# Optimization experiments

Hardware: AMD Instinct MI355X
Metric: run time of the kernel (lower is better)

## Reference

```python
import jax, jax.numpy as jnp
import numpy as np

EMBED_DIM = 512
NUM_HEADS = 8
HEAD_DIM = EMBED_DIM // NUM_HEADS


def setup_inputs() -> dict:
    key = jax.random.key(0)
    ks = jax.random.split(key, 6)
    B, S, D = 2, 4096, EMBED_DIM
    scale = 1.0 / np.sqrt(D)
    inputs = jax.random.normal(ks[0], (B, S, D), dtype=jnp.float32)
    Wq = jax.random.normal(ks[1], (D, D), dtype=jnp.float32) * scale
    Wk = jax.random.normal(ks[2], (D, D), dtype=jnp.float32) * scale
    Wv = jax.random.normal(ks[3], (D, D), dtype=jnp.float32) * scale
    Wo = jax.random.normal(ks[4], (D, D), dtype=jnp.float32) * scale
    zeros = jnp.zeros((D,), dtype=jnp.float32)
    return {"inputs": inputs, "Wq": Wq, "bq": zeros, "Wk": Wk, "bk": zeros,
            "Wv": Wv, "bv": zeros, "Wo": Wo, "bo": zeros}


def _split_heads(x, B, S):
    # [B,S,D] -> [B,H,S,hd]
    return x.reshape(B, S, NUM_HEADS, HEAD_DIM).transpose(0, 2, 1, 3)


def reference(inputs, Wq, bq, Wk, bk, Wv, bv, Wo, bo):
    B, S, D = inputs.shape
    q = _split_heads(inputs @ Wq + bq, B, S)
    k = _split_heads(inputs @ Wk + bk, B, S)
    v = _split_heads(inputs @ Wv + bv, B, S)
    scale = 1.0 / jnp.sqrt(jnp.asarray(HEAD_DIM, dtype=inputs.dtype))
    # full [B,H,S,S] score matrix, as in the original naive SDPA
    scores = jnp.einsum('bhqd,bhkd->bhqk', q, k) * scale
    weights = jax.nn.softmax(scores, axis=-1)
    attn = jnp.einsum('bhqk,bhkd->bhqd', weights, v)
    attn = attn.transpose(0, 2, 1, 3).reshape(B, S, D)
    return attn @ Wo + bo
```

## Files before the change

### kernel.cpp

```cpp
#include <hip/hip_runtime.h>
#include <hip/hip_bf16.h>
#include <stdint.h>


typedef __bf16 bf16x8 __attribute__((ext_vector_type(8)));
typedef float f32x4 __attribute__((ext_vector_type(4)));

using as1_void = __attribute__((address_space(1))) void;
using as3_void = __attribute__((address_space(3))) void;

__device__ __forceinline__ void gload16(const void* g, void* l) {
    __builtin_amdgcn_global_load_lds((const as1_void*)g, (as3_void*)l, 16, 0, 0);
}

__device__ __forceinline__ f32x4 mfma16(bf16x8 a, bf16x8 b, f32x4 c) {
    return __builtin_amdgcn_mfma_f32_16x16x32_bf16(a, b, c, 0, 0, 0);
}

__device__ __forceinline__ uint32_t pkbf(float a, float b) {
    union { __hip_bfloat16 h[2]; uint32_t u; } r;
    r.h[0] = __float2bfloat16(a);
    r.h[1] = __float2bfloat16(b);
    return r.u;
}

__global__ void cvt_x(const float* __restrict__ in, __hip_bfloat16* __restrict__ out, int n) {
    int i = (blockIdx.x * 256 + threadIdx.x) * 4;
    if (i >= n) return;
    float4 v = *reinterpret_cast<const float4*>(in + i);
    union { __hip_bfloat16 h[4]; uint2 u; } r;
    r.h[0] = __float2bfloat16(v.x);
    r.h[1] = __float2bfloat16(v.y);
    r.h[2] = __float2bfloat16(v.z);
    r.h[3] = __float2bfloat16(v.w);
    *reinterpret_cast<uint2*>(out + i) = r.u;
}

__global__ void cvt_wt(const float* __restrict__ w0, const float* __restrict__ w1,
                       const float* __restrict__ w2, const float* __restrict__ w3,
                       __hip_bfloat16* __restrict__ o0, __hip_bfloat16* __restrict__ o1,
                       __hip_bfloat16* __restrict__ o2, __hip_bfloat16* __restrict__ o3) {
    const float* W; __hip_bfloat16* O;
    switch (blockIdx.z) {
        case 0: W = w0; O = o0; break;
        case 1: W = w1; O = o1; break;
        case 2: W = w2; O = o2; break;
        default: W = w3; O = o3; break;
    }
    __shared__ float t[32][33];
    int n0 = blockIdx.x * 32, k0 = blockIdx.y * 32;
    int tx = threadIdx.x, ty = threadIdx.y;
    for (int j = 0; j < 4; ++j)
        t[ty + 8 * j][tx] = W[(size_t)(k0 + ty + 8 * j) * 512 + n0 + tx];
    __syncthreads();
    for (int j = 0; j < 4; ++j)
        O[(size_t)(n0 + ty + 8 * j) * 512 + k0 + tx] = __float2bfloat16(t[tx][ty + 8 * j]);
}

__global__ __launch_bounds__(256, 2) void gemm_qkv(
    const __hip_bfloat16* __restrict__ A, const __hip_bfloat16* __restrict__ Bt,
    const float* __restrict__ bq, const float* __restrict__ bk, const float* __restrict__ bv,
    __hip_bfloat16* __restrict__ Qb, __hip_bfloat16* __restrict__ Kb,
    __hip_bfloat16* __restrict__ Vtb, float qs)
{
    const int K = 512;
    __shared__ __hip_bfloat16 Abuf[128 * 32];
    __shared__ __hip_bfloat16 Bbuf[128 * 32];
    const int tid = threadIdx.x, w = tid >> 6, lane = tid & 63;
    const int col = lane & 15, quad = lane >> 4;
    const int wr = w >> 1, wc = w & 1;
    const int tileN = blockIdx.x * 128, tileM = blockIdx.y * 128;

    f32x4 acc[4][4] = {};

    for (int k0 = 0; k0 < K; k0 += 32) {
        for (int i = 0; i < 2; ++i) {
            int g = w * 2 + i;
            int chunk = g * 64 + lane;
            int row = chunk >> 2, c8 = chunk & 3;
            gload16(A + (size_t)(tileM + row) * K + k0 + c8 * 8, Abuf + g * 512);
            gload16(Bt + (size_t)(tileN + row) * K + k0 + c8 * 8, Bbuf + g * 512);
        }
        __syncthreads();
        bf16x8 af[4], bfr[4];
        for (int mt = 0; mt < 4; ++mt)
            af[mt] = *reinterpret_cast<const bf16x8*>(Abuf + (wr * 64 + mt * 16 + col) * 32 + quad * 8);
        for (int nt = 0; nt < 4; ++nt)
            bfr[nt] = *reinterpret_cast<const bf16x8*>(Bbuf + (wc * 64 + nt * 16 + col) * 32 + quad * 8);
        for (int mt = 0; mt < 4; ++mt)
            for (int nt = 0; nt < 4; ++nt)
                acc[mt][nt] = mfma16(af[mt], bfr[nt], acc[mt][nt]);
        __syncthreads();
    }

    const int seg = (tileN + wc * 64) >> 9;
    const float* bias = (seg == 0) ? bq : (seg == 1) ? bk : bv;
    const float scale = (seg == 0) ? qs : 1.0f;
    __hip_bfloat16* outp = (seg == 0) ? Qb : (seg == 1) ? Kb : Vtb;

    for (int mt = 0; mt < 4; ++mt) {
        for (int nt = 0; nt < 4; ++nt) {
            int n = tileN + wc * 64 + nt * 16 + col;
            int nn = n & 511, h = nn >> 6, d = nn & 63;
            float bn = bias[nn];
            for (int r = 0; r < 4; ++r) {
                int m = tileM + wr * 64 + mt * 16 + quad * 4 + r;
                int b = m >> 12, s = m & 4095;
                float v = (acc[mt][nt][r] + bn) * scale;
                size_t off;
                if (seg < 2) off = (((size_t)(b * 8 + h) * 4096 + s) << 6) + d;
                else         off = (((size_t)(b * 8 + h) * 64 + d) << 12) + s;
                outp[off] = __float2bfloat16(v);
            }
        }
    }
}

__global__ __launch_bounds__(256, 2) void gemm_out(
    const __hip_bfloat16* __restrict__ A, const __hip_bfloat16* __restrict__ Bt,
    const float* __restrict__ bias, float* __restrict__ out)
{
    const int N = 512, K = 512;
    __shared__ __hip_bfloat16 Abuf[128 * 32];
    __shared__ __hip_bfloat16 Bbuf[128 * 32];
    const int tid = threadIdx.x, w = tid >> 6, lane = tid & 63;
    const int col = lane & 15, quad = lane >> 4;
    const int wr = w >> 1, wc = w & 1;
    const int tileN = blockIdx.x * 128, tileM = blockIdx.y * 128;

    f32x4 acc[4][4] = {};

    for (int k0 = 0; k0 < K; k0 += 32) {
        for (int i = 0; i < 2; ++i) {
            int g = w * 2 + i;
            int chunk = g * 64 + lane;
            int row = chunk >> 2, c8 = chunk & 3;
            gload16(A + (size_t)(tileM + row) * K + k0 + c8 * 8, Abuf + g * 512);
            gload16(Bt + (size_t)(tileN + row) * K + k0 + c8 * 8, Bbuf + g * 512);
        }
        __syncthreads();
        bf16x8 af[4], bfr[4];
        for (int mt = 0; mt < 4; ++mt)
            af[mt] = *reinterpret_cast<const bf16x8*>(Abuf + (wr * 64 + mt * 16 + col) * 32 + quad * 8);
        for (int nt = 0; nt < 4; ++nt)
            bfr[nt] = *reinterpret_cast<const bf16x8*>(Bbuf + (wc * 64 + nt * 16 + col) * 32 + quad * 8);
        for (int mt = 0; mt < 4; ++mt)
            for (int nt = 0; nt < 4; ++nt)
                acc[mt][nt] = mfma16(af[mt], bfr[nt], acc[mt][nt]);
        __syncthreads();
    }

    for (int mt = 0; mt < 4; ++mt) {
        for (int nt = 0; nt < 4; ++nt) {
            int n = tileN + wc * 64 + nt * 16 + col;
            float bn = bias[n];
            for (int r = 0; r < 4; ++r) {
                int m = tileM + wr * 64 + mt * 16 + quad * 4 + r;
                out[(size_t)m * N + n] = acc[mt][nt][r] + bn;
            }
        }
    }
}

__global__ __launch_bounds__(256) void flash(
    const __hip_bfloat16* __restrict__ Q,
    const __hip_bfloat16* __restrict__ Kq,
    const __hip_bfloat16* __restrict__ Vt,
    __hip_bfloat16* __restrict__ attnb)
{
    __shared__ __hip_bfloat16 KT[2][4096];
    __shared__ __hip_bfloat16 VB[2][4096];
    __shared__ uint32_t TB[4][1024];

    const int bh = blockIdx.y, b = bh >> 3, h = bh & 7;
    const int tid = threadIdx.x, w = tid >> 6, lane = tid & 63;
    const int col = lane & 15, quad = lane >> 4;
    const int q0 = blockIdx.x * 128 + w * 32;
    const int c7 = col & 7;

    const __hip_bfloat16* Qh = Q + (size_t)bh * 4096 * 64;
    const __hip_bfloat16* Kh = Kq + (size_t)bh * 4096 * 64;
    const __hip_bfloat16* Vh = Vt + (size_t)bh * 64 * 4096;

    bf16x8 aq[2][2];
    for (int qh = 0; qh < 2; ++qh)
        for (int ks = 0; ks < 2; ++ks)
            aq[qh][ks] = *reinterpret_cast<const bf16x8*>(
                Qh + (size_t)(q0 + qh * 16 + col) * 64 + ks * 32 + quad * 8);

    const __hip_bfloat16* ksrc[2];
    const __hip_bfloat16* vsrc[2];
    int ldsoff[2];
    for (int i = 0; i < 2; ++i) {
        int c = i * 256 + tid;
        int row = c >> 3, s8 = (c & 7) ^ (row & 7);
        ksrc[i] = Kh + row * 64 + s8 * 8;
        vsrc[i] = Vh + (size_t)row * 4096 + s8 * 8;
        ldsoff[i] = (i * 256 + w * 64) * 8;
    }

    bf16x8 ones;
    for (int j = 0; j < 8; ++j) ones[j] = (__bf16)1.0f;

    f32x4 o[4][2] = {};
    f32x4 accl[2] = {};

    uint32_t* TBw = &TB[w][0];

    for (int i = 0; i < 2; ++i) {
        gload16(ksrc[i], &KT[0][ldsoff[i]]);
        gload16(vsrc[i], &VB[0][ldsoff[i]]);
    }
    __syncthreads();

    for (int kt = 0; kt < 64; ++kt) {
        const int p = kt & 1;
        if (kt < 63) {
            for (int i = 0; i < 2; ++i) {
                gload16(ksrc[i] + (size_t)(kt + 1) * 4096, &KT[1 - p][ldsoff[i]]);
                gload16(vsrc[i] + (size_t)(kt + 1) * 64,   &VB[1 - p][ldsoff[i]]);
            }
        }

        f32x4 sc[4][2] = {};
        for (int ks = 0; ks < 2; ++ks)
            for (int kg = 0; kg < 4; ++kg) {
                bf16x8 ak = *reinterpret_cast<const bf16x8*>(
                    &KT[p][(kg * 16 + col) * 64 + (((ks * 4 + quad) ^ c7) << 3)]);
                for (int qh = 0; qh < 2; ++qh)
                    sc[kg][qh] = mfma16(ak, aq[qh][ks], sc[kg][qh]);
            }

        for (int kg = 0; kg < 4; ++kg)
            for (int qh = 0; qh < 2; ++qh) {
                f32x4 v = sc[kg][qh];
                uint32_t u0 = pkbf(__builtin_amdgcn_exp2f(v[0]), __builtin_amdgcn_exp2f(v[1]));
                uint32_t u1 = pkbf(__builtin_amdgcn_exp2f(v[2]), __builtin_amdgcn_exp2f(v[3]));
                int q = qh * 16 + col;
                int base = q * 32 + (((kg * 2 + (quad >> 1)) ^ c7) << 2) + ((quad & 1) * 2);
                TBw[base]     = u0;
                TBw[base + 1] = u1;
            }

        bf16x8 bp[2][2];
        for (int qh = 0; qh < 2; ++qh)
            for (int ks = 0; ks < 2; ++ks) {
                int q = qh * 16 + col;
                bp[qh][ks] = *reinterpret_cast<const bf16x8*>(
                    &TBw[q * 32 + (((ks * 4 + quad) ^ c7) << 2)]);
            }

        for (int ks = 0; ks < 2; ++ks) {
            for (int dt = 0; dt < 4; ++dt) {
                bf16x8 av = *reinterpret_cast<const bf16x8*>(
                    &VB[p][(dt * 16 + col) * 64 + (((ks * 4 + quad) ^ c7) << 3)]);
                for (int qh = 0; qh < 2; ++qh)
                    o[dt][qh] = mfma16(av, bp[qh][ks], o[dt][qh]);
            }
            for (int qh = 0; qh < 2; ++qh)
                accl[qh] = mfma16(ones, bp[qh][ks], accl[qh]);
        }

        __syncthreads();
    }

    for (int qh = 0; qh < 2; ++qh) {
        float inv = 1.0f / accl[qh][0];
        int s = q0 + qh * 16 + col;
        __hip_bfloat16* dst = attnb + ((size_t)b * 4096 + s) * 512 + h * 64 + quad * 4;
        for (int dt = 0; dt < 4; ++dt) {
            union { __hip_bfloat16 hh[4]; ushort4 v4; } pk;
            for (int r = 0; r < 4; ++r)
                pk.hh[r] = __float2bfloat16(o[dt][qh][r] * inv);
            *reinterpret_cast<ushort4*>(dst + dt * 16) = pk.v4;
        }
    }
}

extern "C" void kernel_launch(void* const* d_in, const int* in_sizes, int n_in,
                              void* d_out, int out_size, void* d_ws, size_t ws_size,
                              hipStream_t stream) {
    const float* X  = (const float*)d_in[0];
    const float* Wq = (const float*)d_in[1];
    const float* bq = (const float*)d_in[2];
    const float* Wk = (const float*)d_in[3];
    const float* bk = (const float*)d_in[4];
    const float* Wv = (const float*)d_in[5];
    const float* bv = (const float*)d_in[6];
    const float* Wo = (const float*)d_in[7];
    const float* bo = (const float*)d_in[8];
    float* out = (float*)d_out;

    char* ws = (char*)d_ws;
    __hip_bfloat16* Xb  = (__hip_bfloat16*)(ws);
    __hip_bfloat16* Wqt = (__hip_bfloat16*)(ws + ((size_t)8 << 20));
    __hip_bfloat16* Wkt = Wqt + 512 * 512;
    __hip_bfloat16* Wvt = Wkt + 512 * 512;
    __hip_bfloat16* Wot = Wvt + 512 * 512;
    __hip_bfloat16* Qb  = (__hip_bfloat16*)(ws + ((size_t)10 << 20));
    __hip_bfloat16* Kb  = (__hip_bfloat16*)(ws + ((size_t)18 << 20));
    __hip_bfloat16* Vtb = (__hip_bfloat16*)(ws + ((size_t)26 << 20));
    __hip_bfloat16* Atb = (__hip_bfloat16*)(ws + ((size_t)34 << 20));

    const int M = 8192, K = 512;

    cvt_x<<<4096, 256, 0, stream>>>(X, Xb, M * K);
    cvt_wt<<<dim3(16, 16, 4), dim3(32, 8), 0, stream>>>(Wq, Wk, Wv, Wo, Wqt, Wkt, Wvt, Wot);

    const float qs = 0.125f * 1.4426950408889634f;
    gemm_qkv<<<dim3(12, 64), 256, 0, stream>>>(Xb, Wqt, bq, bk, bv, Qb, Kb, Vtb, qs);

    flash<<<dim3(32, 16), 256, 0, stream>>>(Qb, Kb, Vtb, Atb);

    gemm_out<<<dim3(4, 64), 256, 0, stream>>>(Atb, Wot, bo, out);
}
```

Measured before the change: 238.3 us.

## Software-pipeline flash QK^T, merge convert kernels, vectorize GEMM epilogues, retile output GEMM

The flash loop is restructured so the QK^T MFMAs for the next K tile are issued while the current tile's softmax exponentials and PV products run. K is prefetched two tiles ahead and LDS addresses are precomputed, with the loop unrolled by a macro. The input and weight conversion kernels become one launch, and bf16 packing switches to a cheaper round-and-permute helper. GEMM epilogues swap MFMA operand order so each lane writes vectorized rows, and the output GEMM uses 128x64 tiles to launch more blocks. The risks are higher register pressure from the doubled score buffers and the packing helper's rounding differing slightly from round-to-nearest-even.

```diff
diff --git a/kernel.cpp b/kernel.cpp
--- a/kernel.cpp
+++ b/kernel.cpp
@@ -17,44 +17,43 @@
     return __builtin_amdgcn_mfma_f32_16x16x32_bf16(a, b, c, 0, 0, 0);
 }
 
-__device__ __forceinline__ uint32_t pkbf(float a, float b) {
-    union { __hip_bfloat16 h[2]; uint32_t u; } r;
-    r.h[0] = __float2bfloat16(a);
-    r.h[1] = __float2bfloat16(b);
-    return r.u;
-}
-
-__global__ void cvt_x(const float* __restrict__ in, __hip_bfloat16* __restrict__ out, int n) {
-    int i = (blockIdx.x * 256 + threadIdx.x) * 4;
-    if (i >= n) return;
-    float4 v = *reinterpret_cast<const float4*>(in + i);
-    union { __hip_bfloat16 h[4]; uint2 u; } r;
-    r.h[0] = __float2bfloat16(v.x);
-    r.h[1] = __float2bfloat16(v.y);
-    r.h[2] = __float2bfloat16(v.z);
-    r.h[3] = __float2bfloat16(v.w);
-    *reinterpret_cast<uint2*>(out + i) = r.u;
-}
-
-__global__ void cvt_wt(const float* __restrict__ w0, const float* __restrict__ w1,
-                       const float* __restrict__ w2, const float* __restrict__ w3,
-                       __hip_bfloat16* __restrict__ o0, __hip_bfloat16* __restrict__ o1,
-                       __hip_bfloat16* __restrict__ o2, __hip_bfloat16* __restrict__ o3) {
-    const float* W; __hip_bfloat16* O;
-    switch (blockIdx.z) {
-        case 0: W = w0; O = o0; break;
-        case 1: W = w1; O = o1; break;
-        case 2: W = w2; O = o2; break;
-        default: W = w3; O = o3; break;
-    }
+__device__ __forceinline__ uint32_t pk2(float a, float b) {
+    uint32_t ua = __builtin_bit_cast(uint32_t, a) + 0x8000u;
+    uint32_t ub = __builtin_bit_cast(uint32_t, b) + 0x8000u;
+    return __builtin_amdgcn_perm(ub, ua, 0x07060302u);
+}
+
+__global__ void cvt_all(const float* __restrict__ X, __hip_bfloat16* __restrict__ Xb,
+                        const float* __restrict__ w0, const float* __restrict__ w1,
+                        const float* __restrict__ w2, const float* __restrict__ w3,
+                        __hip_bfloat16* __restrict__ o0, __hip_bfloat16* __restrict__ o1,
+                        __hip_bfloat16* __restrict__ o2, __hip_bfloat16* __restrict__ o3) {
     __shared__ float t[32][33];
-    int n0 = blockIdx.x * 32, k0 = blockIdx.y * 32;
-    int tx = threadIdx.x, ty = threadIdx.y;
-    for (int j = 0; j < 4; ++j)
-        t[ty + 8 * j][tx] = W[(size_t)(k0 + ty + 8 * j) * 512 + n0 + tx];
-    __syncthreads();
-    for (int j = 0; j < 4; ++j)
-        O[(size_t)(n0 + ty + 8 * j) * 512 + k0 + tx] = __float2bfloat16(t[tx][ty + 8 * j]);
+    const int bid = blockIdx.x, tid = threadIdx.x;
+    if (bid < 1024) {
+        const float* W; __hip_bfloat16* O;
+        switch (bid >> 8) {
+            case 0: W = w0; O = o0; break;
+            case 1: W = w1; O = o1; break;
+            case 2: W = w2; O = o2; break;
+            default: W = w3; O = o3; break;
+        }
+        int rem = bid & 255;
+        int n0 = (rem & 15) * 32, k0 = (rem >> 4) * 32;
+        int tx = tid & 31, ty = tid >> 5;
+        for (int j = 0; j < 4; ++j)
+            t[ty + 8 * j][tx] = W[(size_t)(k0 + ty + 8 * j) * 512 + n0 + tx];
+        __syncthreads();
+        for (int j = 0; j < 4; ++j)
+            O[(size_t)(n0 + ty + 8 * j) * 512 + k0 + tx] = __float2bfloat16(t[tx][ty + 8 * j]);
+    } else {
+        int i = ((bid - 1024) * 256 + tid) * 4;
+        float4 v = *reinterpret_cast<const float4*>(X + i);
+        uint2 u;
+        u.x = pk2(v.x, v.y);
+        u.y = pk2(v.z, v.w);
+        *reinterpret_cast<uint2*>(Xb + i) = u;
+    }
 }
 
 __global__ __launch_bounds__(256, 2) void gemm_qkv(
@@ -70,6 +69,7 @@
     const int col = lane & 15, quad = lane >> 4;
     const int wr = w >> 1, wc = w & 1;
     const int tileN = blockIdx.x * 128, tileM = blockIdx.y * 128;
+    const int seg = tileN >> 9;
 
     f32x4 acc[4][4] = {};
 
@@ -87,30 +87,50 @@
             af[mt] = *reinterpret_cast<const bf16x8*>(Abuf + (wr * 64 + mt * 16 + col) * 32 + quad * 8);
         for (int nt = 0; nt < 4; ++nt)
             bfr[nt] = *reinterpret_cast<const bf16x8*>(Bbuf + (wc * 64 + nt * 16 + col) * 32 + quad * 8);
-        for (int mt = 0; mt < 4; ++mt)
-            for (int nt = 0; nt < 4; ++nt)
-                acc[mt][nt] = mfma16(af[mt], bfr[nt], acc[mt][nt]);
-        __syncthreads();
-    }
-
-    const int seg = (tileN + wc * 64) >> 9;
-    const float* bias = (seg == 0) ? bq : (seg == 1) ? bk : bv;
-    const float scale = (seg == 0) ? qs : 1.0f;
-    __hip_bfloat16* outp = (seg == 0) ? Qb : (seg == 1) ? Kb : Vtb;
-
-    for (int mt = 0; mt < 4; ++mt) {
+        if (seg < 2) {
+            for (int mt = 0; mt < 4; ++mt)
+                for (int nt = 0; nt < 4; ++nt)
+                    acc[nt][mt] = mfma16(bfr[nt], af[mt], acc[nt][mt]);
+        } else {
+            for (int mt = 0; mt < 4; ++mt)
+                for (int nt = 0; nt < 4; ++nt)
+                    acc[mt][nt] = mfma16(af[mt], bfr[nt], acc[mt][nt]);
+        }
+        __syncthreads();
+    }
+
+    const int nbase = (tileN & 511) + wc * 64;
+    if (seg < 2) {
+        const float* bias = (seg == 0) ? bq : bk;
+        const float scale = (seg == 0) ? qs : 1.0f;
+        __hip_bfloat16* outp = (seg == 0) ? Qb : Kb;
         for (int nt = 0; nt < 4; ++nt) {
-            int n = tileN + wc * 64 + nt * 16 + col;
-            int nn = n & 511, h = nn >> 6, d = nn & 63;
-            float bn = bias[nn];
-            for (int r = 0; r < 4; ++r) {
-                int m = tileM + wr * 64 + mt * 16 + quad * 4 + r;
+            int nn0 = nbase + nt * 16 + quad * 4;
+            f32x4 b4 = *reinterpret_cast<const f32x4*>(bias + nn0);
+            int h = nn0 >> 6, d0 = nn0 & 63;
+            for (int mt = 0; mt < 4; ++mt) {
+                int m = tileM + wr * 64 + mt * 16 + col;
                 int b = m >> 12, s = m & 4095;
-                float v = (acc[mt][nt][r] + bn) * scale;
-                size_t off;
-                if (seg < 2) off = (((size_t)(b * 8 + h) * 4096 + s) << 6) + d;
-                else         off = (((size_t)(b * 8 + h) * 64 + d) << 12) + s;
-                outp[off] = __float2bfloat16(v);
+                f32x4 v = (acc[nt][mt] + b4) * scale;
+                uint2 u;
+                u.x = pk2(v[0], v[1]);
+                u.y = pk2(v[2], v[3]);
+                *reinterpret_cast<uint2*>(outp + (((size_t)(b * 8 + h) * 4096 + s) << 6) + d0) = u;
+            }
+        }
+    } else {
+        for (int nt = 0; nt < 4; ++nt) {
+            int nn0 = nbase + nt * 16 + col;
+            int h = nn0 >> 6, d = nn0 & 63;
+            float bn = bv[nn0];
+            for (int mt = 0; mt < 4; ++mt) {
+                int s0 = tileM + wr * 64 + mt * 16 + quad * 4;
+                int b = s0 >> 12;
+                f32x4 v = acc[mt][nt];
+                uint2 u;
+                u.x = pk2(v[0] + bn, v[1] + bn);
+                u.y = pk2(v[2] + bn, v[3] + bn);
+                *reinterpret_cast<uint2*>(Vtb + (((size_t)(b * 8 + h) * 64 + d) << 12) + (s0 & 4095)) = u;
             }
         }
     }
@@ -120,15 +140,14 @@
     const __hip_bfloat16* __restrict__ A, const __hip_bfloat16* __restrict__ Bt,
     const float* __restrict__ bias, float* __restrict__ out)
 {
-    const int N = 512, K = 512;
+    const int K = 512;
     __shared__ __hip_bfloat16 Abuf[128 * 32];
-    __shared__ __hip_bfloat16 Bbuf[128 * 32];
+    __shared__ __hip_bfloat16 Bbuf[64 * 32];
     const int tid = threadIdx.x, w = tid >> 6, lane = tid & 63;
     const int col = lane & 15, quad = lane >> 4;
-    const int wr = w >> 1, wc = w & 1;
-    const int tileN = blockIdx.x * 128, tileM = blockIdx.y * 128;
-
-    f32x4 acc[4][4] = {};
+    const int tileN = blockIdx.x * 64, tileM = blockIdx.y * 128;
+
+    f32x4 acc[4][2] = {};
 
     for (int k0 = 0; k0 < K; k0 += 32) {
         for (int i = 0; i < 2; ++i) {
@@ -136,28 +155,30 @@
             int chunk = g * 64 + lane;
             int row = chunk >> 2, c8 = chunk & 3;
             gload16(A + (size_t)(tileM + row) * K + k0 + c8 * 8, Abuf + g * 512);
-            gload16(Bt + (size_t)(tileN + row) * K + k0 + c8 * 8, Bbuf + g * 512);
-        }
-        __syncthreads();
-        bf16x8 af[4], bfr[4];
-        for (int mt = 0; mt < 4; ++mt)
-            af[mt] = *reinterpret_cast<const bf16x8*>(Abuf + (wr * 64 + mt * 16 + col) * 32 + quad * 8);
+        }
+        {
+            int row = tid >> 2, c8 = tid & 3;
+            gload16(Bt + (size_t)(tileN + row) * K + k0 + c8 * 8, Bbuf + tid * 8);
+        }
+        __syncthreads();
+        bf16x8 af[2], bfr[4];
+        for (int mt = 0; mt < 2; ++mt)
+            af[mt] = *reinterpret_cast<const bf16x8*>(Abuf + (w * 32 + mt * 16 + col) * 32 + quad * 8);
         for (int nt = 0; nt < 4; ++nt)
-            bfr[nt] = *reinterpret_cast<const bf16x8*>(Bbuf + (wc * 64 + nt * 16 + col) * 32 + quad * 8);
-        for (int mt = 0; mt < 4; ++mt)
+            bfr[nt] = *reinterpret_cast<const bf16x8*>(Bbuf + (nt * 16 + col) * 32 + quad * 8);
+        for (int mt = 0; mt < 2; ++mt)
             for (int nt = 0; nt < 4; ++nt)
-                acc[mt][nt] = mfma16(af[mt], bfr[nt], acc[mt][nt]);
-        __syncthreads();
-    }
-
-    for (int mt = 0; mt < 4; ++mt) {
-        for (int nt = 0; nt < 4; ++nt) {
-            int n = tileN + wc * 64 + nt * 16 + col;
-            float bn = bias[n];
-            for (int r = 0; r < 4; ++r) {
-                int m = tileM + wr * 64 + mt * 16 + quad * 4 + r;
-                out[(size_t)m * N + n] = acc[mt][nt][r] + bn;
-            }
+                acc[nt][mt] = mfma16(bfr[nt], af[mt], acc[nt][mt]);
+        __syncthreads();
+    }
+
+    for (int nt = 0; nt < 4; ++nt) {
+        int n0 = tileN + nt * 16 + quad * 4;
+        f32x4 b4 = *reinterpret_cast<const f32x4*>(bias + n0);
+        for (int mt = 0; mt < 2; ++mt) {
+            int m = tileM + w * 32 + mt * 16 + col;
+            f32x4 v = acc[nt][mt] + b4;
+            *reinterpret_cast<f32x4*>(out + (size_t)m * 512 + n0) = v;
         }
     }
 }
@@ -204,75 +225,132 @@
 
     f32x4 o[4][2] = {};
     f32x4 accl[2] = {};
-
-    uint32_t* TBw = &TB[w][0];
-
-    for (int i = 0; i < 2; ++i) {
-        gload16(ksrc[i], &KT[0][ldsoff[i]]);
-        gload16(vsrc[i], &VB[0][ldsoff[i]]);
-    }
+    f32x4 sc[2][4][2];
+    const f32x4 z4 = {0.f, 0.f, 0.f, 0.f};
+
+    const char* KTb = (const char*)&KT[0][0];
+    const char* VBb = (const char*)&VB[0][0];
+    char* TBb = (char*)&TB[w][0];
+    const int ra0 = col * 128 + ((quad ^ c7) * 16);
+    const int ra1 = col * 128 + (((4 + quad) ^ c7) * 16);
+    int two[4];
+    {
+        int basew = col * 128 + (((quad >> 1) ^ (c7 & 1)) * 16) + ((quad & 1) * 8);
+        for (int j = 0; j < 4; ++j) two[j] = basew + ((j ^ (c7 >> 1)) * 32);
+    }
+
+    gload16(ksrc[0], &KT[0][ldsoff[0]]);
+    gload16(ksrc[1], &KT[0][ldsoff[1]]);
+    gload16(vsrc[0], &VB[0][ldsoff[0]]);
+    gload16(vsrc[1], &VB[0][ldsoff[1]]);
+    gload16(ksrc[0] + 4096, &KT[1][ldsoff[0]]);
+    gload16(ksrc[1] + 4096, &KT[1][ldsoff[1]]);
     __syncthreads();
 
-    for (int kt = 0; kt < 64; ++kt) {
-        const int p = kt & 1;
-        if (kt < 63) {
-            for (int i = 0; i < 2; ++i) {
-                gload16(ksrc[i] + (size_t)(kt + 1) * 4096, &KT[1 - p][ldsoff[i]]);
-                gload16(vsrc[i] + (size_t)(kt + 1) * 64,   &VB[1 - p][ldsoff[i]]);
-            }
-        }
-
-        f32x4 sc[4][2] = {};
-        for (int ks = 0; ks < 2; ++ks)
-            for (int kg = 0; kg < 4; ++kg) {
-                bf16x8 ak = *reinterpret_cast<const bf16x8*>(
-                    &KT[p][(kg * 16 + col) * 64 + (((ks * 4 + quad) ^ c7) << 3)]);
-                for (int qh = 0; qh < 2; ++qh)
-                    sc[kg][qh] = mfma16(ak, aq[qh][ks], sc[kg][qh]);
-            }
-
+    for (int kg = 0; kg < 4; ++kg) {
+        bf16x8 ak = *reinterpret_cast<const bf16x8*>(KTb + kg * 2048 + ra0);
+        for (int qh = 0; qh < 2; ++qh)
+            sc[0][kg][qh] = mfma16(ak, aq[qh][0], z4);
+    }
+    for (int kg = 0; kg < 4; ++kg) {
+        bf16x8 ak = *reinterpret_cast<const bf16x8*>(KTb + kg * 2048 + ra1);
+        for (int qh = 0; qh < 2; ++qh)
+            sc[0][kg][qh] = mfma16(ak, aq[qh][1], sc[0][kg][qh]);
+    }
+    __syncthreads();
+
+#define FLASH_BODY(KT_, P_)                                                      \
+    {                                                                            \
+        const int kt_ = (KT_);                                                   \
+        int kk = kt_ + 2; if (kk > 63) kk = 63;                                  \
+        gload16(ksrc[0] + (size_t)kk * 4096, &KT[(P_)][ldsoff[0]]);              \
+        gload16(ksrc[1] + (size_t)kk * 4096, &KT[(P_)][ldsoff[1]]);              \
+        gload16(vsrc[0] + (size_t)(kt_ + 1) * 64, &VB[1 - (P_)][ldsoff[0]]);     \
+        gload16(vsrc[1] + (size_t)(kt_ + 1) * 64, &VB[1 - (P_)][ldsoff[1]]);     \
+                            \
+        for (int kg = 0; kg < 4; ++kg)                                           \
+            for (int qh = 0; qh < 2; ++qh) {                                     \
+                f32x4 v = sc[(P_)][kg][qh];                                      \
+                uint2 u;                                                         \
+                u.x = pk2(__builtin_amdgcn_exp2f(v[0]),                          \
+                          __builtin_amdgcn_exp2f(v[1]));                         \
+                u.y = pk2(__builtin_amdgcn_exp2f(v[2]),                          \
+                          __builtin_amdgcn_exp2f(v[3]));                         \
+                *reinterpret_cast<uint2*>(TBb + qh * 2048 + two[kg]) = u;        \
+            }                                                                    \
+                                             \
+        for (int kg = 0; kg < 4; ++kg) {                                         \
+            bf16x8 ak = *reinterpret_cast<const bf16x8*>(                        \
+                KTb + (1 - (P_)) * 8192 + kg * 2048 + ra0);                      \
+            for (int qh = 0; qh < 2; ++qh)                                       \
+                sc[1 - (P_)][kg][qh] = mfma16(ak, aq[qh][0], z4);                \
+        }                                                                        \
+        for (int kg = 0; kg < 4; ++kg) {                                         \
+            bf16x8 ak = *reinterpret_cast<const bf16x8*>(                        \
+                KTb + (1 - (P_)) * 8192 + kg * 2048 + ra1);                      \
+            for (int qh = 0; qh < 2; ++qh)                                       \
+                sc[1 - (P_)][kg][qh] = mfma16(ak, aq[qh][1], sc[1 - (P_)][kg][qh]); \
+        }                                                                        \
+                                                                     \
+        bf16x8 bp[2][2];                                                         \
+        for (int qh = 0; qh < 2; ++qh) {                                         \
+            bp[qh][0] = *reinterpret_cast<const bf16x8*>(TBb + qh * 2048 + ra0); \
+            bp[qh][1] = *reinterpret_cast<const bf16x8*>(TBb + qh * 2048 + ra1); \
+        }                                                                        \
+        for (int ks = 0; ks < 2; ++ks) {                                         \
+            for (int dt = 0; dt < 4; ++dt) {                                     \
+                bf16x8 av = *reinterpret_cast<const bf16x8*>(                    \
+                    VBb + (P_) * 8192 + dt * 2048 + (ks ? ra1 : ra0));           \
+                for (int qh = 0; qh < 2; ++qh)                                   \
+                    o[dt][qh] = mfma16(av, bp[qh][ks], o[dt][qh]);               \
+            }                                                                    \
+            accl[0] = mfma16(ones, bp[0][ks], accl[0]);                          \
+            accl[1] = mfma16(ones, bp[1][ks], accl[1]);                          \
+        }                                                                        \
+        __syncthreads();                                                         \
+    }
+
+    FLASH_BODY(0, 0)
+    for (int kth = 0; kth < 31; ++kth) {
+        FLASH_BODY(2 * kth + 1, 1)
+        FLASH_BODY(2 * kth + 2, 0)
+    }
+    {
         for (int kg = 0; kg < 4; ++kg)
             for (int qh = 0; qh < 2; ++qh) {
-                f32x4 v = sc[kg][qh];
-                uint32_t u0 = pkbf(__builtin_amdgcn_exp2f(v[0]), __builtin_amdgcn_exp2f(v[1]));
-                uint32_t u1 = pkbf(__builtin_amdgcn_exp2f(v[2]), __builtin_amdgcn_exp2f(v[3]));
-                int q = qh * 16 + col;
-                int base = q * 32 + (((kg * 2 + (quad >> 1)) ^ c7) << 2) + ((quad & 1) * 2);
-                TBw[base]     = u0;
-                TBw[base + 1] = u1;
+                f32x4 v = sc[1][kg][qh];
+                uint2 u;
+                u.x = pk2(__builtin_amdgcn_exp2f(v[0]), __builtin_amdgcn_exp2f(v[1]));
+                u.y = pk2(__builtin_amdgcn_exp2f(v[2]), __builtin_amdgcn_exp2f(v[3]));
+                *reinterpret_cast<uint2*>(TBb + qh * 2048 + two[kg]) = u;
             }
-
         bf16x8 bp[2][2];
-        for (int qh = 0; qh < 2; ++qh)
-            for (int ks = 0; ks < 2; ++ks) {
-                int q = qh * 16 + col;
-                bp[qh][ks] = *reinterpret_cast<const bf16x8*>(
-                    &TBw[q * 32 + (((ks * 4 + quad) ^ c7) << 2)]);
-            }
-
+        for (int qh = 0; qh < 2; ++qh) {
+            bp[qh][0] = *reinterpret_cast<const bf16x8*>(TBb + qh * 2048 + ra0);
+            bp[qh][1] = *reinterpret_cast<const bf16x8*>(TBb + qh * 2048 + ra1);
+        }
         for (int ks = 0; ks < 2; ++ks) {
             for (int dt = 0; dt < 4; ++dt) {
                 bf16x8 av = *reinterpret_cast<const bf16x8*>(
-                    &VB[p][(dt * 16 + col) * 64 + (((ks * 4 + quad) ^ c7) << 3)]);
+                    VBb + 8192 + dt * 2048 + (ks ? ra1 : ra0));
                 for (int qh = 0; qh < 2; ++qh)
                     o[dt][qh] = mfma16(av, bp[qh][ks], o[dt][qh]);
             }
-            for (int qh = 0; qh < 2; ++qh)
-                accl[qh] = mfma16(ones, bp[qh][ks], accl[qh]);
-        }
-
-        __syncthreads();
-    }
+            accl[0] = mfma16(ones, bp[0][ks], accl[0]);
+            accl[1] = mfma16(ones, bp[1][ks], accl[1]);
+        }
+    }
+#undef FLASH_BODY
 
     for (int qh = 0; qh < 2; ++qh) {
         float inv = 1.0f / accl[qh][0];
         int s = q0 + qh * 16 + col;
         __hip_bfloat16* dst = attnb + ((size_t)b * 4096 + s) * 512 + h * 64 + quad * 4;
         for (int dt = 0; dt < 4; ++dt) {
-            union { __hip_bfloat16 hh[4]; ushort4 v4; } pk;
-            for (int r = 0; r < 4; ++r)
-                pk.hh[r] = __float2bfloat16(o[dt][qh][r] * inv);
-            *reinterpret_cast<ushort4*>(dst + dt * 16) = pk.v4;
+            uint2 u;
+            u.x = pk2(o[dt][qh][0] * inv, o[dt][qh][1] * inv);
+            u.y = pk2(o[dt][qh][2] * inv, o[dt][qh][3] * inv);
+            *reinterpret_cast<uint2*>(dst + dt * 16) = u;
         }
     }
 }
@@ -302,15 +380,10 @@
     __hip_bfloat16* Vtb = (__hip_bfloat16*)(ws + ((size_t)26 << 20));
     __hip_bfloat16* Atb = (__hip_bfloat16*)(ws + ((size_t)34 << 20));
 
-    const int M = 8192, K = 512;
-
-    cvt_x<<<4096, 256, 0, stream>>>(X, Xb, M * K);
-    cvt_wt<<<dim3(16, 16, 4), dim3(32, 8), 0, stream>>>(Wq, Wk, Wv, Wo, Wqt, Wkt, Wvt, Wot);
+    cvt_all<<<5120, 256, 0, stream>>>(X, Xb, Wq, Wk, Wv, Wo, Wqt, Wkt, Wvt, Wot);
 
     const float qs = 0.125f * 1.4426950408889634f;
     gemm_qkv<<<dim3(12, 64), 256, 0, stream>>>(Xb, Wqt, bq, bk, bv, Qb, Kb, Vtb, qs);
-
     flash<<<dim3(32, 16), 256, 0, stream>>>(Qb, Kb, Vtb, Atb);
-
-    gemm_out<<<dim3(4, 64), 256, 0, stream>>>(Atb, Wot, bo, out);
-}
+    gemm_out<<<dim3(8, 64), 256, 0, stream>>>(Atb, Wot, bo, out);
+}
```

Result: faster. 227.5 us (-4.5%).
